# Performance work log

Hardware: AMD Instinct MI355X
Metric: run time of the kernel (lower is better)

The kernel has to match this reference:

```python
import jax, jax.numpy as jnp
import numpy as np

B, S, E, H = 1, 2048, 512, 8
D = E // H
N = B * S
WIN_HALF = 32  # attention_window 64 -> +/-32
ALPHA = 0.1
LN_EPS = 1e-12
NEG_INF = -1e9


def _build_window_edges():
    # windowed graph: dst i attends to src j with |i-j| <= WIN_HALF, within each batch block
    i = np.arange(S)
    offs = np.arange(-WIN_HALF, WIN_HALF + 1)
    src = i[:, None] + offs[None, :]
    dst = np.broadcast_to(i[:, None], src.shape)
    valid = (src >= 0) & (src < S)
    src, dst = src[valid], dst[valid]
    srcs, dsts = [], []
    for b in range(B):
        srcs.append(src + b * S)
        dsts.append(dst + b * S)
    return (np.concatenate(srcs).astype(np.int32),
            np.concatenate(dsts).astype(np.int32))


def setup_inputs() -> dict:
    key = jax.random.key(0)
    ks = jax.random.split(key, 12)
    sc = 1.0 / np.sqrt(E)
    src_np, dst_np = _build_window_edges()
    return {
        "hidden_states": jax.random.normal(ks[0], (B, S, E), dtype=jnp.float32),
        "attention_mask": jnp.zeros((B, S), dtype=jnp.float32),
        "edge_src": jnp.asarray(src_np),
        "edge_dst": jnp.asarray(dst_np),
        "Wq": jax.random.normal(ks[1], (E, E), dtype=jnp.float32) * sc,
        "bq": jnp.zeros((E,), dtype=jnp.float32),
        "Wk": jax.random.normal(ks[2], (E, E), dtype=jnp.float32) * sc,
        "bk": jnp.zeros((E,), dtype=jnp.float32),
        "Wv": jax.random.normal(ks[3], (E, E), dtype=jnp.float32) * sc,
        "bv": jnp.zeros((E,), dtype=jnp.float32),
        "Wo": jax.random.normal(ks[4], (E, E), dtype=jnp.float32) * sc,
        "bo": jnp.zeros((E,), dtype=jnp.float32),
        "ln_g": jnp.ones((E,), dtype=jnp.float32),
        "ln_b": jnp.zeros((E,), dtype=jnp.float32),
    }


def reference(hidden_states, attention_mask, edge_src, edge_dst,
              Wq, bq, Wk, bk, Wv, bv, Wo, bo, ln_g, ln_b):
    x = hidden_states  # (B,S,E); node ordering n = b*S + s (matches torch reshape)
    q = ((x @ Wq + bq) / jnp.sqrt(jnp.asarray(D, x.dtype))).reshape(N, H, D)
    k = (x @ Wk + bk).reshape(N, H, D)
    v = (x @ Wv + bv).reshape(N, H, D)

    mask = (attention_mask >= 0).reshape(N)  # bool per node

    # u_dot_v('k','q','score'): per-edge, per-head dot product
    score = jnp.einsum('ehd,ehd->eh', k[edge_src], q[edge_dst])  # (Eg,H)
    score = jnp.where(mask[edge_src][:, None], score, NEG_INF)

    # edge_softmax over incoming edges of each destination node
    smax = jax.ops.segment_max(score, edge_dst, num_segments=N)
    p = jnp.exp(score - smax[edge_dst])
    denom = jax.ops.segment_sum(p, edge_dst, num_segments=N)
    p = p / denom[edge_dst]  # (Eg,H)

    # 5 diffusion steps: h <- A h, blended with residual v (dropout off in eval)
    h = v
    for _ in range(5):
        m = h[edge_src] * p[:, :, None]                      # u_mul_e
        h = jax.ops.segment_sum(m, edge_dst, num_segments=N)  # sum('m','h')
        h = (1.0 - ALPHA) * h + ALPHA * v

    attn = h.reshape(B, S, E)

    # DiffuserSelfOutput: dense -> residual add -> LayerNorm
    y = attn @ Wo + bo + hidden_states
    mu = y.mean(-1, keepdims=True)
    var = ((y - mu) ** 2).mean(-1, keepdims=True)
    out = (y - mu) * jax.lax.rsqrt(var + LN_EPS) * ln_g + ln_b
    return out
```

## Files before the change

kernel.cpp:

```cpp
#include <hip/hip_runtime.h>
#include <math.h>

#define S_LEN 2048
#define E_DIM 512
#define NE (S_LEN * E_DIM)
#define H_NUM 8
#define WH 32
#define NOFF 65
#define PROW (H_NUM * NOFF)
#define PN (S_LEN * PROW)

typedef float f32x4 __attribute__((ext_vector_type(4)));
typedef short short8 __attribute__((ext_vector_type(8)));

__device__ __forceinline__ unsigned short f2bf(float f) {
    union { float f; unsigned u; } cv; cv.f = f;
    unsigned u = cv.u;
    u += 0x7fffu + ((u >> 16) & 1u);
    return (unsigned short)(u >> 16);
}
__device__ __forceinline__ unsigned pk2(float x, float y) {
    return (unsigned)f2bf(x) | ((unsigned)f2bf(y) << 16);
}

__device__ __forceinline__ void mfma_gemm_f32(
    const float* __restrict__ A, const float* __restrict__ W,
    const float* __restrict__ bias, float* __restrict__ C,
    float scale, int m0, int n0)
{
    __shared__ unsigned short As[64 * 40];
    __shared__ unsigned short Bs[64 * 40];
    const int tid = threadIdx.x;
    const int lane = tid & 63, wave = tid >> 6;
    const int quad = lane >> 4, l16 = lane & 15;
    const int wr = (wave >> 1) * 32, wc = (wave & 1) * 32;
    const int ar = tid >> 2, ac = (tid & 3) * 8;
    const int bn = tid & 63, bk0 = (tid >> 6) * 8;

    f32x4 acc00 = {0.f,0.f,0.f,0.f}, acc01 = acc00, acc10 = acc00, acc11 = acc00;

    for (int kk = 0; kk < E_DIM; kk += 32) {
        float4 a0 = *(const float4*)(A + (size_t)(m0 + ar) * E_DIM + kk + ac);
        float4 a1 = *(const float4*)(A + (size_t)(m0 + ar) * E_DIM + kk + ac + 4);
        float b[8];
#pragma unroll
        for (int j = 0; j < 8; ++j)
            b[j] = W[(size_t)(kk + bk0 + j) * E_DIM + n0 + bn];
        __syncthreads();
        uint4 ap; ap.x = pk2(a0.x, a0.y); ap.y = pk2(a0.z, a0.w);
        ap.z = pk2(a1.x, a1.y); ap.w = pk2(a1.z, a1.w);
        *(uint4*)(As + ar * 40 + ac) = ap;
        uint4 bp; bp.x = pk2(b[0], b[1]); bp.y = pk2(b[2], b[3]);
        bp.z = pk2(b[4], b[5]); bp.w = pk2(b[6], b[7]);
        *(uint4*)(Bs + bn * 40 + bk0) = bp;
        __syncthreads();
        short8 fa0 = *(const short8*)(As + (wr + l16) * 40 + quad * 8);
        short8 fa1 = *(const short8*)(As + (wr + 16 + l16) * 40 + quad * 8);
        short8 fb0 = *(const short8*)(Bs + (wc + l16) * 40 + quad * 8);
        short8 fb1 = *(const short8*)(Bs + (wc + 16 + l16) * 40 + quad * 8);
        acc00 = __builtin_amdgcn_mfma_f32_16x16x32_bf16(fa0, fb0, acc00, 0, 0, 0);
        acc01 = __builtin_amdgcn_mfma_f32_16x16x32_bf16(fa0, fb1, acc01, 0, 0, 0);
        acc10 = __builtin_amdgcn_mfma_f32_16x16x32_bf16(fa1, fb0, acc10, 0, 0, 0);
        acc11 = __builtin_amdgcn_mfma_f32_16x16x32_bf16(fa1, fb1, acc11, 0, 0, 0);
    }

#pragma unroll
    for (int mi = 0; mi < 2; ++mi) {
#pragma unroll
        for (int ni = 0; ni < 2; ++ni) {
            f32x4 a = (mi == 0) ? ((ni == 0) ? acc00 : acc01)
                                : ((ni == 0) ? acc10 : acc11);
            int n = n0 + wc + ni * 16 + l16;
            float bval = bias[n];
#pragma unroll
            for (int r = 0; r < 4; ++r) {
                int m = m0 + wr + mi * 16 + quad * 4 + r;
                C[(size_t)m * E_DIM + n] = (a[r] + bval) * scale;
            }
        }
    }
}

__global__ __launch_bounds__(256)
void qkv_gemm(const float* __restrict__ x,
              const float* __restrict__ Wq, const float* __restrict__ bq,
              const float* __restrict__ Wk, const float* __restrict__ bk,
              const float* __restrict__ Wv, const float* __restrict__ bv,
              const float* __restrict__ Wo, unsigned short* __restrict__ WoT,
              float* __restrict__ q, float* __restrict__ k, float* __restrict__ v)
{
    if (blockIdx.z == 3) {
        if (blockIdx.y >= 8) return;
        __shared__ float tile[64][65];
        const int tid = threadIdx.x;
        const int n0 = blockIdx.x * 64, k0 = blockIdx.y * 64;
        const int r = tid >> 2;
#pragma unroll
        for (int s = 0; s < 4; ++s) {
            int c4 = (tid & 3) + 4 * s;
            float4 vv = ((const float4*)(Wo + (size_t)(k0 + r) * E_DIM + n0))[c4];
            tile[r][c4 * 4 + 0] = vv.x; tile[r][c4 * 4 + 1] = vv.y;
            tile[r][c4 * 4 + 2] = vv.z; tile[r][c4 * 4 + 3] = vv.w;
        }
        __syncthreads();
#pragma unroll
        for (int s = 0; s < 4; ++s) {
            int c4 = (tid & 3) + 4 * s;
            ushort4 o;
            o.x = f2bf(tile[c4 * 4 + 0][r]);
            o.y = f2bf(tile[c4 * 4 + 1][r]);
            o.z = f2bf(tile[c4 * 4 + 2][r]);
            o.w = f2bf(tile[c4 * 4 + 3][r]);
            *(ushort4*)(WoT + (size_t)(n0 + r) * E_DIM + k0 + c4 * 4) = o;
        }
        return;
    }
    const float* W; const float* b; float* o; float sc;
    if (blockIdx.z == 0)      { W = Wq; b = bq; o = q; sc = 0.125f; }
    else if (blockIdx.z == 1) { W = Wk; b = bk; o = k; sc = 1.0f; }
    else                      { W = Wv; b = bv; o = v; sc = 1.0f; }
    mfma_gemm_f32(x, W, b, o, sc, blockIdx.y * 64, blockIdx.x * 64);
}

#define SDN 32
__global__ __launch_bounds__(256)
void scores_d1(const float* __restrict__ q, const float* __restrict__ k,
               const float* __restrict__ v, const float* __restrict__ amask,
               float* __restrict__ P, float* __restrict__ hA)
{
    const int i0 = blockIdx.x * SDN;
    const int h  = blockIdx.y;
    const int tid = threadIdx.x;
    __shared__ float ks[96 * 68];
    __shared__ float am[96];
    __shared__ float sc[SDN * 66];
    __shared__ float smx[SDN], sidn[SDN];
    __shared__ float ps[SDN * NOFF];

    for (int e = tid; e < 96 * 16; e += 256) {
        int lr = e >> 4, c4 = e & 15;
        int j = i0 - WH + lr;
        int jc = min(max(j, 0), S_LEN - 1);
        *(float4*)(ks + lr * 68 + c4 * 4) =
            *(const float4*)(k + (size_t)jc * E_DIM + h * 64 + c4 * 4);
    }
    if (tid < 96) {
        int j = i0 - WH + tid;
        am[tid] = (j >= 0 && j < S_LEN) ? amask[j] : -1.0f;
    }

    const int dst = tid >> 3;
    const int og  = tid & 7;
    float4 qreg[16];
    {
        const float4* qrow = (const float4*)(q + (size_t)(i0 + dst) * E_DIM + h * 64);
#pragma unroll
        for (int t = 0; t < 16; ++t) qreg[t] = qrow[t];
    }
    __syncthreads();

    for (int off = og; off < NOFF; off += 8) {
        int j = i0 + dst + off - WH;
        float s;
        if (j < 0 || j >= S_LEN) {
            s = -INFINITY;
        } else {
            int lr = dst + off;
            const float4* kr = (const float4*)(ks + lr * 68);
            float acc = 0.f;
#pragma unroll
            for (int t = 0; t < 16; ++t) {
                float4 a = qreg[t], bb = kr[t];
                acc += a.x * bb.x + a.y * bb.y + a.z * bb.z + a.w * bb.w;
            }
            s = (am[lr] >= 0.f) ? acc : -1e9f;
        }
        sc[dst * 66 + off] = s;
    }
    __syncthreads();

    for (int e = tid; e < 96 * 16; e += 256) {
        int lr = e >> 4, c4 = e & 15;
        int j = i0 - WH + lr;
        int jc = min(max(j, 0), S_LEN - 1);
        *(float4*)(ks + lr * 68 + c4 * 4) =
            *(const float4*)(v + (size_t)jc * E_DIM + h * 64 + c4 * 4);
    }
    if (tid < SDN) {
        float mx = -INFINITY;
        for (int o = 0; o < NOFF; ++o) mx = fmaxf(mx, sc[tid * 66 + o]);
        float dn = 0.f;
        for (int o = 0; o < NOFF; ++o) dn += expf(sc[tid * 66 + o] - mx);
        smx[tid] = mx; sidn[tid] = 1.f / dn;
    }
    __syncthreads();

    for (int e = tid; e < SDN * NOFF; e += 256) {
        int d = e / NOFF, off = e - d * NOFF;
        float pv = expf(sc[d * 66 + off] - smx[d]) * sidn[d];
        P[(size_t)(i0 + d) * PROW + h * NOFF + off] = pv;
        ps[e] = pv;
    }
    __syncthreads();

    {
        const int ci = tid & 15;
        const int ob = (tid >> 4) * 2;
        float4 a0 = {0,0,0,0}, a1 = a0;
        for (int lr = ob; lr < ob + 66; ++lr) {
            float4 hval = *(const float4*)(ks + lr * 68 + ci * 4);
            int o0 = lr - ob;
            if (o0 <= 64) {
                float p = ps[ob * NOFF + o0];
                a0.x += p * hval.x; a0.y += p * hval.y; a0.z += p * hval.z; a0.w += p * hval.w;
            }
            int o1 = o0 - 1;
            if ((unsigned)o1 <= 64u) {
                float p = ps[(ob + 1) * NOFF + o1];
                a1.x += p * hval.x; a1.y += p * hval.y; a1.z += p * hval.z; a1.w += p * hval.w;
            }
        }
#pragma unroll
        for (int r = 0; r < 2; ++r) {
            float4 a = r ? a1 : a0;
            float4 vv = *(const float4*)(ks + (WH + ob + r) * 68 + ci * 4);
            float4 o;
            o.x = 0.9f * a.x + 0.1f * vv.x;
            o.y = 0.9f * a.y + 0.1f * vv.y;
            o.z = 0.9f * a.z + 0.1f * vv.z;
            o.w = 0.9f * a.w + 0.1f * vv.w;
            *(float4*)(hA + (size_t)(i0 + ob + r) * E_DIM + h * 64 + ci * 4) = o;
        }
    }
}

__global__ __launch_bounds__(512)
void diffuse3m(const float* __restrict__ hin, const float* __restrict__ v,
               const float* __restrict__ P, float* __restrict__ hout)
{
    __shared__ unsigned short inT[64 * 264];
    __shared__ unsigned short m1T[64 * 200];
    __shared__ unsigned short ps[192 * 66];
    unsigned short* m2T = inT;
    const int i0 = blockIdx.x * 64;
    const int h  = blockIdx.y;
    const int c0 = h * 64;
    const int tid  = threadIdx.x;
    const int lane = tid & 63, wave = tid >> 6;
    const int quad = lane >> 4, l16 = lane & 15;

    for (int e = tid; e < 128 * 16; e += 512) {
        int rp = (e >> 4) * 2, c4 = (e & 15) * 4;
        int ja = min(max(i0 - 96 + rp,     0), S_LEN - 1);
        int jb = min(max(i0 - 96 + rp + 1, 0), S_LEN - 1);
        float4 ha = *(const float4*)(hin + (size_t)ja * E_DIM + c0 + c4);
        float4 hb = *(const float4*)(hin + (size_t)jb * E_DIM + c0 + c4);
        *(unsigned*)(inT + (c4 + 0) * 264 + rp) = pk2(ha.x, hb.x);
        *(unsigned*)(inT + (c4 + 1) * 264 + rp) = pk2(ha.y, hb.y);
        *(unsigned*)(inT + (c4 + 2) * 264 + rp) = pk2(ha.z, hb.z);
        *(unsigned*)(inT + (c4 + 3) * 264 + rp) = pk2(ha.w, hb.w);
    }
    for (int e = tid; e < 192 * 33; e += 512) {
        int mr = e / 33, t = e - mr * 33;
        int jc = min(max(i0 - 64 + mr, 0), S_LEN - 1);
        const float* pr = P + (size_t)jc * PROW + h * NOFF;
        if (t < 32)
            *(unsigned*)(ps + mr * 66 + t * 2) = pk2(pr[t * 2], pr[t * 2 + 1]);
        else
            ps[mr * 66 + 64] = f2bf(pr[64]);
    }
    __syncthreads();

#pragma unroll
    for (int uu = 0; uu < 3; ++uu) {
        int u = wave + uu * 8;
        int mtb = (u >> 1) * 16;
        int ntb = (u & 1) * 32;
        f32x4 a0 = {0.f,0.f,0.f,0.f}, a1 = a0;
        int ks0 = mtb >> 5;
        const int m = mtb + l16;
#pragma unroll
        for (int t = 0; t < 3; ++t) {
            int k0q = (ks0 + t) * 32 + quad * 8;
            short8 fa;
#pragma unroll
            for (int j = 0; j < 8; ++j) {
                int idx = k0q + j - m;
                int idc = min(max(idx, 0), 64);
                unsigned short pv = ps[m * 66 + idc];
                fa[j] = ((unsigned)idx <= 64u) ? (short)pv : (short)0;
            }
            short8 fb0 = *(const short8*)(inT + (ntb + l16) * 264 + k0q);
            short8 fb1 = *(const short8*)(inT + (ntb + 16 + l16) * 264 + k0q);
            a0 = __builtin_amdgcn_mfma_f32_16x16x32_bf16(fa, fb0, a0, 0, 0, 0);
            a1 = __builtin_amdgcn_mfma_f32_16x16x32_bf16(fa, fb1, a1, 0, 0, 0);
        }
#pragma unroll
        for (int nt = 0; nt < 2; ++nt) {
            f32x4 a = nt ? a1 : a0;
            int n = ntb + nt * 16 + l16;
            float o[4];
#pragma unroll
            for (int r = 0; r < 4; ++r) {
                int gm = min(max(i0 - 64 + mtb + quad * 4 + r, 0), S_LEN - 1);
                o[r] = 0.9f * a[r] + 0.1f * v[(size_t)gm * E_DIM + c0 + n];
            }
            *(unsigned*)(m1T + n * 200 + mtb + quad * 4)     = pk2(o[0], o[1]);
            *(unsigned*)(m1T + n * 200 + mtb + quad * 4 + 2) = pk2(o[2], o[3]);
        }
    }
    __syncthreads();

#pragma unroll
    for (int uu = 0; uu < 2; ++uu) {
        int u = wave + uu * 8;
        int mtb = (u >> 1) * 16;
        int ntb = (u & 1) * 32;
        f32x4 a0 = {0.f,0.f,0.f,0.f}, a1 = a0;
        int ks0 = mtb >> 5;
        const int m = mtb + l16;
#pragma unroll
        for (int t = 0; t < 3; ++t) {
            int k0q = (ks0 + t) * 32 + quad * 8;
            short8 fa;
#pragma unroll
            for (int j = 0; j < 8; ++j) {
                int idx = k0q + j - m;
                int idc = min(max(idx, 0), 64);
                unsigned short pv = ps[(m + 32) * 66 + idc];
                fa[j] = ((unsigned)idx <= 64u) ? (short)pv : (short)0;
            }
            short8 fb0 = *(const short8*)(m1T + (ntb + l16) * 200 + k0q);
            short8 fb1 = *(const short8*)(m1T + (ntb + 16 + l16) * 200 + k0q);
            a0 = __builtin_amdgcn_mfma_f32_16x16x32_bf16(fa, fb0, a0, 0, 0, 0);
            a1 = __builtin_amdgcn_mfma_f32_16x16x32_bf16(fa, fb1, a1, 0, 0, 0);
        }
#pragma unroll
        for (int nt = 0; nt < 2; ++nt) {
            f32x4 a = nt ? a1 : a0;
            int n = ntb + nt * 16 + l16;
            float o[4];
#pragma unroll
            for (int r = 0; r < 4; ++r) {
                int gm = min(max(i0 - 32 + mtb + quad * 4 + r, 0), S_LEN - 1);
                o[r] = 0.9f * a[r] + 0.1f * v[(size_t)gm * E_DIM + c0 + n];
            }
            *(unsigned*)(m2T + n * 136 + mtb + quad * 4)     = pk2(o[0], o[1]);
            *(unsigned*)(m2T + n * 136 + mtb + quad * 4 + 2) = pk2(o[2], o[3]);
        }
    }
    __syncthreads();

    {
        int u = wave;
        int mtb = (u >> 1) * 16;
        int ntb = (u & 1) * 32;
        f32x4 a0 = {0.f,0.f,0.f,0.f}, a1 = a0;
        int ks0 = mtb >> 5;
        const int m = mtb + l16;
#pragma unroll
        for (int t = 0; t < 3; ++t) {
            int k0q = (ks0 + t) * 32 + quad * 8;
            short8 fa;
#pragma unroll
            for (int j = 0; j < 8; ++j) {
                int idx = k0q + j - m;
                int idc = min(max(idx, 0), 64);
                unsigned short pv = ps[(m + 64) * 66 + idc];
                fa[j] = ((unsigned)idx <= 64u) ? (short)pv : (short)0;
            }
            short8 fb0 = *(const short8*)(m2T + (ntb + l16) * 136 + k0q);
            short8 fb1 = *(const short8*)(m2T + (ntb + 16 + l16) * 136 + k0q);
            a0 = __builtin_amdgcn_mfma_f32_16x16x32_bf16(fa, fb0, a0, 0, 0, 0);
            a1 = __builtin_amdgcn_mfma_f32_16x16x32_bf16(fa, fb1, a1, 0, 0, 0);
        }
#pragma unroll
        for (int nt = 0; nt < 2; ++nt) {
            f32x4 a = nt ? a1 : a0;
            int n = ntb + nt * 16 + l16;
#pragma unroll
            for (int r = 0; r < 4; ++r) {
                int gm = i0 + mtb + quad * 4 + r;
                size_t base = (size_t)gm * E_DIM + c0 + n;
                hout[base] = 0.9f * a[r] + 0.1f * v[base];
            }
        }
    }
}

__global__ __launch_bounds__(512)
void oln3(const float* __restrict__ h4, const float* __restrict__ v,
          const float* __restrict__ P, const unsigned short* __restrict__ WoT,
          const float* __restrict__ bo, const float* __restrict__ x,
          const float* __restrict__ g, const float* __restrict__ lb,
          float* __restrict__ out)
{
    __shared__ unsigned short As[16 * 40];
    __shared__ unsigned short h4T[32 * 96];
    __shared__ unsigned short ps16[8 * 528];
    __shared__ float rsum[8][8], rsq[8][8];
    const int tid = threadIdx.x;
    const int lane = tid & 63, wave = tid >> 6;
    const int quad = lane >> 4, l16 = lane & 15;
    const int m0 = blockIdx.x * 8;

    {
        int col = tid >> 4, r = tid & 15;
        h4T[col * 96 + 80 + r] = 0;
        if (tid < 320) As[320 + tid] = 0;
    }
    for (int e = tid; e < 8 * 260; e += 512) {
        int mr = e / 260, t = e - mr * 260;
        const float* pr = P + (size_t)(m0 + mr) * PROW;
        *(unsigned*)(ps16 + mr * 528 + t * 2) = pk2(pr[t * 2], pr[t * 2 + 1]);
    }

    f32x4 acc[4];
#pragma unroll
    for (int t = 0; t < 4; ++t) acc[t] = (f32x4){0.f,0.f,0.f,0.f};

    for (int kk = 0; kk < E_DIM; kk += 32) {
        const int hd = kk >> 6;
        float4 hv0, hv1;
        {
            int r = tid >> 3, c4 = (tid & 7) * 4;
            int jc = min(max(m0 - 32 + r, 0), S_LEN - 1);
            hv0 = *(const float4*)(h4 + (size_t)jc * E_DIM + kk + c4);
        }
        if (tid < 128) {
            int e = tid + 512;
            int r = e >> 3, c4 = (e & 7) * 4;
            int jc = min(max(m0 - 32 + r, 0), S_LEN - 1);
            hv1 = *(const float4*)(h4 + (size_t)jc * E_DIM + kk + c4);
        }
        __syncthreads();
        {
            int r = tid >> 3, c4 = (tid & 7) * 4;
            h4T[(c4 + 0) * 96 + r] = f2bf(hv0.x);
            h4T[(c4 + 1) * 96 + r] = f2bf(hv0.y);
            h4T[(c4 + 2) * 96 + r] = f2bf(hv0.z);
            h4T[(c4 + 3) * 96 + r] = f2bf(hv0.w);
        }
        if (tid < 128) {
            int e = tid + 512;
            int r = e >> 3, c4 = (e & 7) * 4;
            h4T[(c4 + 0) * 96 + r] = f2bf(hv1.x);
            h4T[(c4 + 1) * 96 + r] = f2bf(hv1.y);
            h4T[(c4 + 2) * 96 + r] = f2bf(hv1.z);
            h4T[(c4 + 3) * 96 + r] = f2bf(hv1.w);
        }
        __syncthreads();

        if (wave < 2) {
            const int ntb = wave * 16;
            const int mrow = min(l16, 7);
            f32x4 ba = {0.f,0.f,0.f,0.f};
#pragma unroll
            for (int t = 0; t < 3; ++t) {
                int k0q = t * 32 + quad * 8;
                short8 fa;
#pragma unroll
                for (int j = 0; j < 8; ++j) {
                    int idx = k0q + j - l16;
                    int idc = min(max(idx, 0), 64);
                    unsigned short pv = ps16[mrow * 528 + hd * NOFF + idc];
                    fa[j] = ((unsigned)idx <= 64u && l16 < 8) ? (short)pv : (short)0;
                }
                short8 fb = *(const short8*)(h4T + (ntb + l16) * 96 + k0q);
                ba = __builtin_amdgcn_mfma_f32_16x16x32_bf16(fa, fb, ba, 0, 0, 0);
            }
            if (quad < 2) {
#pragma unroll
                for (int r = 0; r < 4; ++r) {
                    int m = quad * 4 + r;
                    float vv = v[(size_t)(m0 + m) * E_DIM + kk + ntb + l16];
                    As[m * 40 + ntb + l16] = f2bf(0.9f * ba[r] + 0.1f * vv);
                }
            }
        }
        __syncthreads();

        short8 fa = *(const short8*)(As + l16 * 40 + quad * 8);
#pragma unroll
        for (int nt = 0; nt < 4; ++nt) {
            int n = wave * 64 + nt * 16 + l16;
            short8 fb = *(const short8*)(WoT + (size_t)n * E_DIM + kk + quad * 8);
            acc[nt] = __builtin_amdgcn_mfma_f32_16x16x32_bf16(fa, fb, acc[nt], 0, 0, 0);
        }
    }

    float s[4] = {0.f,0.f,0.f,0.f}, s2[4] = {0.f,0.f,0.f,0.f};
#pragma unroll
    for (int nt = 0; nt < 4; ++nt) {
        int nc = wave * 64 + nt * 16 + l16;
        float bv = bo[nc];
#pragma unroll
        for (int r = 0; r < 4; ++r) {
            int mc = min(quad * 4 + r, 7);
            float vl = acc[nt][r] + bv + x[(size_t)(m0 + mc) * E_DIM + nc];
            acc[nt][r] = vl;
            s[r] += vl; s2[r] += vl * vl;
        }
    }
#pragma unroll
    for (int o = 1; o < 16; o <<= 1) {
#pragma unroll
        for (int r = 0; r < 4; ++r) {
            s[r]  += __shfl_xor(s[r], o, 64);
            s2[r] += __shfl_xor(s2[r], o, 64);
        }
    }
    if (l16 == 0 && quad < 2) {
#pragma unroll
        for (int r = 0; r < 4; ++r) {
            rsum[wave][quad * 4 + r] = s[r];
            rsq[wave][quad * 4 + r]  = s2[r];
        }
    }
    __syncthreads();
    if (quad < 2) {
        float mu[4], rs[4];
#pragma unroll
        for (int r = 0; r < 4; ++r) {
            int rl = quad * 4 + r;
            float tot = 0.f, tot2 = 0.f;
#pragma unroll
            for (int w = 0; w < 8; ++w) { tot += rsum[w][rl]; tot2 += rsq[w][rl]; }
            float m_ = tot * (1.f / 512.f);
            float var = tot2 * (1.f / 512.f) - m_ * m_;
            mu[r] = m_; rs[r] = rsqrtf(var + 1e-12f);
        }
#pragma unroll
        for (int nt = 0; nt < 4; ++nt) {
            int nc = wave * 64 + nt * 16 + l16;
            float gv = g[nc], bbv = lb[nc];
#pragma unroll
            for (int r = 0; r < 4; ++r) {
                int m = m0 + quad * 4 + r;
                out[(size_t)m * E_DIM + nc] = (acc[nt][r] - mu[r]) * rs[r] * gv + bbv;
            }
        }
    }
}

extern "C" void kernel_launch(void* const* d_in, const int* in_sizes, int n_in,
                              void* d_out, int out_size, void* d_ws, size_t ws_size,
                              hipStream_t stream)
{
    const float* x     = (const float*)d_in[0];
    const float* amask = (const float*)d_in[1];
    const float* Wq = (const float*)d_in[4];
    const float* bq = (const float*)d_in[5];
    const float* Wk = (const float*)d_in[6];
    const float* bk = (const float*)d_in[7];
    const float* Wv = (const float*)d_in[8];
    const float* bv = (const float*)d_in[9];
    const float* Wo = (const float*)d_in[10];
    const float* bo = (const float*)d_in[11];
    const float* lng = (const float*)d_in[12];
    const float* lnb = (const float*)d_in[13];
    float* out = (float*)d_out;

    float* ws = (float*)d_ws;
    float* q  = ws;
    float* k  = ws + (size_t)NE;
    float* v  = ws + (size_t)2 * NE;
    float* P  = ws + (size_t)3 * NE;
    float* hA = ws + (size_t)3 * NE + PN;
    float* hB = hA + (size_t)NE;
    unsigned short* WoT = (unsigned short*)(hB + (size_t)NE);

    qkv_gemm<<<dim3(8, 32, 4), 256, 0, stream>>>(x, Wq, bq, Wk, bk, Wv, bv,
                                                 Wo, WoT, q, k, v);

    scores_d1<<<dim3(64, 8), 256, 0, stream>>>(q, k, v, amask, P, hA);

    diffuse3m<<<dim3(32, 8), 512, 0, stream>>>(hA, v, P, hB);

    oln3<<<256, 512, 0, stream>>>(hB, v, P, WoT, bo, x, lng, lnb, out);
}
```

Before: 178.3 us.

## Double rows per block and widen k-chunk in fused output+LayerNorm kernel

The final fused diffusion-step/output-projection/LayerNorm kernel now handles 16 rows per block instead of 8, so the 16-row MFMA tile is fully used rather than half padded. It also processes 128 columns of K per iteration with all 8 waves doing the diffusion MFMA, instead of 32 columns with only 2 waves. This cuts the number of barriers and raises MFMA utilisation and WoT reuse. The cost is half as many blocks (128), which lowers occupancy across CUs, plus more shared memory and registers per block.

```diff
diff --git a/kernel.cpp b/kernel.cpp
--- a/kernel.cpp
+++ b/kernel.cpp
@@ -395,21 +395,22 @@
           const float* __restrict__ g, const float* __restrict__ lb,
           float* __restrict__ out)
 {
-    __shared__ unsigned short As[16 * 40];
-    __shared__ unsigned short h4T[32 * 96];
-    __shared__ unsigned short ps16[8 * 528];
-    __shared__ float rsum[8][8], rsq[8][8];
+    __shared__ unsigned short As[16 * 136];
+    __shared__ unsigned short h4T[128 * 96];
+    __shared__ unsigned short ps16[16 * 528];
+    __shared__ float rsum[8][16], rsq[8][16];
     const int tid = threadIdx.x;
     const int lane = tid & 63, wave = tid >> 6;
     const int quad = lane >> 4, l16 = lane & 15;
-    const int m0 = blockIdx.x * 8;
+    const int m0 = blockIdx.x * 16;
 
     {
-        int col = tid >> 4, r = tid & 15;
-        h4T[col * 96 + 80 + r] = 0;
-        if (tid < 320) As[320 + tid] = 0;
-    }
-    for (int e = tid; e < 8 * 260; e += 512) {
+        int col = tid >> 2, r = tid & 3;
+#pragma unroll
+        for (int t = 0; t < 4; ++t)
+            h4T[col * 96 + 80 + r * 4 + t] = 0;
+    }
+    for (int e = tid; e < 16 * 260; e += 512) {
         int mr = e / 260, t = e - mr * 260;
         const float* pr = P + (size_t)(m0 + mr) * PROW;
         *(unsigned*)(ps16 + mr * 528 + t * 2) = pk2(pr[t * 2], pr[t * 2 + 1]);
@@ -419,41 +420,30 @@
 #pragma unroll
     for (int t = 0; t < 4; ++t) acc[t] = (f32x4){0.f,0.f,0.f,0.f};
 
-    for (int kk = 0; kk < E_DIM; kk += 32) {
-        const int hd = kk >> 6;
-        float4 hv0, hv1;
+    for (int kk = 0; kk < E_DIM; kk += 128) {
+        float4 hv[5];
+#pragma unroll
+        for (int t = 0; t < 5; ++t) {
+            int e = tid + t * 512;
+            int r = e >> 5, c4 = e & 31;
+            int jc = min(max(m0 - 32 + r, 0), S_LEN - 1);
+            hv[t] = *(const float4*)(h4 + (size_t)jc * E_DIM + kk + c4 * 4);
+        }
+        __syncthreads();
+#pragma unroll
+        for (int t = 0; t < 5; ++t) {
+            int e = tid + t * 512;
+            int r = e >> 5, c4 = (e & 31) * 4;
+            h4T[(c4 + 0) * 96 + r] = f2bf(hv[t].x);
+            h4T[(c4 + 1) * 96 + r] = f2bf(hv[t].y);
+            h4T[(c4 + 2) * 96 + r] = f2bf(hv[t].z);
+            h4T[(c4 + 3) * 96 + r] = f2bf(hv[t].w);
+        }
+        __syncthreads();
+
         {
-            int r = tid >> 3, c4 = (tid & 7) * 4;
-            int jc = min(max(m0 - 32 + r, 0), S_LEN - 1);
-            hv0 = *(const float4*)(h4 + (size_t)jc * E_DIM + kk + c4);
-        }
-        if (tid < 128) {
-            int e = tid + 512;
-            int r = e >> 3, c4 = (e & 7) * 4;
-            int jc = min(max(m0 - 32 + r, 0), S_LEN - 1);
-            hv1 = *(const float4*)(h4 + (size_t)jc * E_DIM + kk + c4);
-        }
-        __syncthreads();
-        {
-            int r = tid >> 3, c4 = (tid & 7) * 4;
-            h4T[(c4 + 0) * 96 + r] = f2bf(hv0.x);
-            h4T[(c4 + 1) * 96 + r] = f2bf(hv0.y);
-            h4T[(c4 + 2) * 96 + r] = f2bf(hv0.z);
-            h4T[(c4 + 3) * 96 + r] = f2bf(hv0.w);
-        }
-        if (tid < 128) {
-            int e = tid + 512;
-            int r = e >> 3, c4 = (e & 7) * 4;
-            h4T[(c4 + 0) * 96 + r] = f2bf(hv1.x);
-            h4T[(c4 + 1) * 96 + r] = f2bf(hv1.y);
-            h4T[(c4 + 2) * 96 + r] = f2bf(hv1.z);
-            h4T[(c4 + 3) * 96 + r] = f2bf(hv1.w);
-        }
-        __syncthreads();
-
-        if (wave < 2) {
             const int ntb = wave * 16;
-            const int mrow = min(l16, 7);
+            const int hd = (kk + ntb) >> 6;
             f32x4 ba = {0.f,0.f,0.f,0.f};
 #pragma unroll
             for (int t = 0; t < 3; ++t) {
@@ -463,29 +453,30 @@
                 for (int j = 0; j < 8; ++j) {
                     int idx = k0q + j - l16;
                     int idc = min(max(idx, 0), 64);
-                    unsigned short pv = ps16[mrow * 528 + hd * NOFF + idc];
-                    fa[j] = ((unsigned)idx <= 64u && l16 < 8) ? (short)pv : (short)0;
+                    unsigned short pv = ps16[l16 * 528 + hd * NOFF + idc];
+                    fa[j] = ((unsigned)idx <= 64u) ? (short)pv : (short)0;
                 }
                 short8 fb = *(const short8*)(h4T + (ntb + l16) * 96 + k0q);
                 ba = __builtin_amdgcn_mfma_f32_16x16x32_bf16(fa, fb, ba, 0, 0, 0);
             }
-            if (quad < 2) {
-#pragma unroll
-                for (int r = 0; r < 4; ++r) {
-                    int m = quad * 4 + r;
-                    float vv = v[(size_t)(m0 + m) * E_DIM + kk + ntb + l16];
-                    As[m * 40 + ntb + l16] = f2bf(0.9f * ba[r] + 0.1f * vv);
-                }
+#pragma unroll
+            for (int r = 0; r < 4; ++r) {
+                int m = quad * 4 + r;
+                float vv = v[(size_t)(m0 + m) * E_DIM + kk + ntb + l16];
+                As[m * 136 + ntb + l16] = f2bf(0.9f * ba[r] + 0.1f * vv);
             }
         }
         __syncthreads();
 
-        short8 fa = *(const short8*)(As + l16 * 40 + quad * 8);
-#pragma unroll
-        for (int nt = 0; nt < 4; ++nt) {
-            int n = wave * 64 + nt * 16 + l16;
-            short8 fb = *(const short8*)(WoT + (size_t)n * E_DIM + kk + quad * 8);
-            acc[nt] = __builtin_amdgcn_mfma_f32_16x16x32_bf16(fa, fb, acc[nt], 0, 0, 0);
+#pragma unroll
+        for (int kq = 0; kq < 4; ++kq) {
+            short8 fa = *(const short8*)(As + l16 * 136 + kq * 32 + quad * 8);
+#pragma unroll
+            for (int nt = 0; nt < 4; ++nt) {
+                int n = wave * 64 + nt * 16 + l16;
+                short8 fb = *(const short8*)(WoT + (size_t)n * E_DIM + kk + kq * 32 + quad * 8);
+                acc[nt] = __builtin_amdgcn_mfma_f32_16x16x32_bf16(fa, fb, acc[nt], 0, 0, 0);
+            }
         }
     }
 
@@ -496,8 +487,8 @@
         float bv = bo[nc];
 #pragma unroll
         for (int r = 0; r < 4; ++r) {
-            int mc = min(quad * 4 + r, 7);
-            float vl = acc[nt][r] + bv + x[(size_t)(m0 + mc) * E_DIM + nc];
+            int m = m0 + quad * 4 + r;
+            float vl = acc[nt][r] + bv + x[(size_t)m * E_DIM + nc];
             acc[nt][r] = vl;
             s[r] += vl; s2[r] += vl * vl;
         }
@@ -510,7 +501,7 @@
             s2[r] += __shfl_xor(s2[r], o, 64);
         }
     }
-    if (l16 == 0 && quad < 2) {
+    if (l16 == 0) {
 #pragma unroll
         for (int r = 0; r < 4; ++r) {
             rsum[wave][quad * 4 + r] = s[r];
@@ -518,27 +509,25 @@
         }
     }
     __syncthreads();
-    if (quad < 2) {
-        float mu[4], rs[4];
+    float mu[4], rs[4];
+#pragma unroll
+    for (int r = 0; r < 4; ++r) {
+        int rl = quad * 4 + r;
+        float tot = 0.f, tot2 = 0.f;
+#pragma unroll
+        for (int w = 0; w < 8; ++w) { tot += rsum[w][rl]; tot2 += rsq[w][rl]; }
+        float m_ = tot * (1.f / 512.f);
+        float var = tot2 * (1.f / 512.f) - m_ * m_;
+        mu[r] = m_; rs[r] = rsqrtf(var + 1e-12f);
+    }
+#pragma unroll
+    for (int nt = 0; nt < 4; ++nt) {
+        int nc = wave * 64 + nt * 16 + l16;
+        float gv = g[nc], bbv = lb[nc];
 #pragma unroll
         for (int r = 0; r < 4; ++r) {
-            int rl = quad * 4 + r;
-            float tot = 0.f, tot2 = 0.f;
-#pragma unroll
-            for (int w = 0; w < 8; ++w) { tot += rsum[w][rl]; tot2 += rsq[w][rl]; }
-            float m_ = tot * (1.f / 512.f);
-            float var = tot2 * (1.f / 512.f) - m_ * m_;
-            mu[r] = m_; rs[r] = rsqrtf(var + 1e-12f);
-        }
-#pragma unroll
-        for (int nt = 0; nt < 4; ++nt) {
-            int nc = wave * 64 + nt * 16 + l16;
-            float gv = g[nc], bbv = lb[nc];
-#pragma unroll
-            for (int r = 0; r < 4; ++r) {
-                int m = m0 + quad * 4 + r;
-                out[(size_t)m * E_DIM + nc] = (acc[nt][r] - mu[r]) * rs[r] * gv + bbv;
-            }
+            int m = m0 + quad * 4 + r;
+            out[(size_t)m * E_DIM + nc] = (acc[nt][r] - mu[r]) * rs[r] * gv + bbv;
         }
     }
 }
@@ -577,5 +566,5 @@
 
     diffuse3m<<<dim3(32, 8), 512, 0, stream>>>(hA, v, P, hB);
 
-    oln3<<<256, 512, 0, stream>>>(hB, v, P, WoT, bo, x, lng, lnb, out);
-}
+    oln3<<<128, 512, 0, stream>>>(hB, v, P, WoT, bo, x, lng, lnb, out);
+}
```

After: 182.0 us. 2.1% more time.
